# Optimization experiments

Hardware: AMD Instinct MI355X
Metric: run time of the kernel (lower is better)

## Reference

```python
import jax, jax.numpy as jnp
import numpy as np

ORDER = 2
C_IN = 32   # per-hop feature dim d
C_OUT = 64


def setup_inputs() -> dict:
    key = jax.random.key(0)
    k = jax.random.split(key, 6)
    b, num_n, num_m, d, t = 2, 512, 256, C_IN, 128
    feat_context = jax.random.normal(k[0], (b, num_n, d, t), dtype=jnp.float32)
    feat_target = jax.random.normal(k[1], (b, num_m, d, t), dtype=jnp.float32)
    adj = jax.random.uniform(k[2], (b, ORDER, num_m, num_n), dtype=jnp.float32)
    missing_mask_context = jax.random.randint(k[3], (b, t, num_n), 0, 2).astype(jnp.float32)
    c_cat = (ORDER + 1) * d  # 96
    W_mlp = jax.random.normal(k[4], (C_OUT, c_cat), dtype=jnp.float32) / np.sqrt(c_cat)
    b_mlp = jax.random.normal(k[5], (C_OUT,), dtype=jnp.float32) * 0.01
    return {"feat_context": feat_context, "feat_target": feat_target, "adj": adj,
            "missing_mask_context": missing_mask_context, "W_mlp": W_mlp, "b_mlp": b_mlp}


def _aggregate(fc_btnd, ft_btmd, adj_bmn, mask_btn):
    # mask out missing context nodes, per (batch, time)
    a = adj_bmn[:, None, :, :] * (1.0 - mask_btn[:, :, None, :])   # [b,t,m,n]
    norm = a / (jnp.sum(a, axis=-1, keepdims=True) + 1.0)          # [b,t,m,n]
    # residual + adjacency-weighted neighbor sum (batched matmul instead of [b,t,m,n,d] blow-up)
    agg = ft_btmd + jnp.einsum('btmn,btnd->btmd', norm, fc_btnd)   # [b,t,m,d]
    return agg


def reference(feat_context, feat_target, adj, missing_mask_context, W_mlp, b_mlp):
    # feat_context: [b,n,d,t], feat_target: [b,m,d,t], adj: [b,k,m,n], mask: [b,t,n]
    fc = jnp.transpose(feat_context, (0, 3, 1, 2))  # [b,t,n,d]
    ft = jnp.transpose(feat_target, (0, 3, 1, 2))   # [b,t,m,d]
    outs = [feat_target]
    for i in range(ORDER):
        agg = _aggregate(fc, ft, adj[:, i], missing_mask_context)      # [b,t,m,d]
        outs.append(jnp.transpose(agg, (0, 2, 3, 1)))                  # [b,m,d,t]
    out = jnp.concatenate(outs, axis=2)  # [b,m,(order+1)*d,t]
    # 1x1 conv over the feature channel dim + ReLU (dropout is identity at eval)
    y = jnp.einsum('bmct,oc->bmot', out, W_mlp) + b_mlp[None, None, :, None]
    return jax.nn.relu(y)  # [b,m,c_out,t]
```

## Files before the change

### kernel.cpp

```cpp
#include <hip/hip_runtime.h>
#include <cstdint>
#include <cstddef>


using shortx8 = __attribute__((ext_vector_type(8))) short;
using floatx4 = __attribute__((ext_vector_type(4))) float;

__device__ __forceinline__ float b2f(unsigned short u) {
    union { unsigned int i; float f; } v; v.i = ((unsigned int)u) << 16; return v.f;
}
__device__ __forceinline__ unsigned short f2b(float f) {
    union { float f; unsigned int i; } v; v.f = f;
    unsigned int x = v.i;
    return (unsigned short)((x + 0x7FFFu + ((x >> 16) & 1u)) >> 16);
}
__device__ __forceinline__ void gl_lds16(const unsigned short* g, unsigned short* l) {
    __builtin_amdgcn_global_load_lds(
        (const __attribute__((address_space(1))) unsigned int*)g,
        (__attribute__((address_space(3))) unsigned int*)l, 16, 0, 0);
}

__global__ void k_adj(const float* __restrict__ adj, const float* __restrict__ W,
                      unsigned short* __restrict__ adjb, unsigned short* __restrict__ Wb) {
    if (blockIdx.x == 512) {
        for (int e = threadIdx.x; e < 2048; e += 256) {
            int o = e >> 5, d = e & 31;
            float w1 = W[o * 96 + d], w2 = W[o * 96 + 32 + d], w3 = W[o * 96 + 64 + d];
            Wb[e]        = f2b(w1 + w2 + w3);
            Wb[2048 + e] = f2b(w2);
            Wb[4096 + e] = f2b(w3);
        }
        return;
    }
    int i4 = (blockIdx.x * 256 + threadIdx.x) * 4;
    float4 v = *(const float4*)(adj + i4);
    ushort4 o;
    o.x = f2b(v.x); o.y = f2b(v.y); o.z = f2b(v.z); o.w = f2b(v.w);
    *(ushort4*)(adjb + i4) = o;
}

__global__ void k_g(const float* __restrict__ fc, const float* __restrict__ mask,
                    unsigned short* __restrict__ gt) {
    const int jb = blockIdx.x, nb = blockIdx.y, b = blockIdx.z;
    const int tid = threadIdx.x;
    const int n0 = nb * 32;
    const int r = tid >> 3, c4 = (tid & 7) * 4;
    if (jb >= 128) {
        const int t0 = (jb - 128) * 32;
        float4 mv = *(const float4*)(mask + ((size_t)b * 128 + t0 + r) * 512 + n0 + c4);
        ushort4 o;
        o.x = f2b(1.f - mv.x); o.y = f2b(1.f - mv.y);
        o.z = f2b(1.f - mv.z); o.w = f2b(1.f - mv.w);
        *(ushort4*)(gt + ((size_t)b * 4224 + 4096 + t0 + r) * 512 + n0 + c4) = o;
        return;
    }
    const int j0 = jb * 32;
    const int t0 = j0 & 127;
    __shared__ float wls[32][33];
    __shared__ unsigned short tls[32][34];
    {
        float4 mv = *(const float4*)(mask + ((size_t)b * 128 + t0 + r) * 512 + n0 + c4);
        wls[r][c4 + 0] = 1.f - mv.x; wls[r][c4 + 1] = 1.f - mv.y;
        wls[r][c4 + 2] = 1.f - mv.z; wls[r][c4 + 3] = 1.f - mv.w;
    }
    float4 fv = *(const float4*)(fc + ((size_t)b * 512 + n0 + r) * 4096 + j0 + c4);
    __syncthreads();
    tls[c4 + 0][r] = f2b(fv.x * wls[c4 + 0][r]);
    tls[c4 + 1][r] = f2b(fv.y * wls[c4 + 1][r]);
    tls[c4 + 2][r] = f2b(fv.z * wls[c4 + 2][r]);
    tls[c4 + 3][r] = f2b(fv.w * wls[c4 + 3][r]);
    __syncthreads();
    ushort4 o;
    o.x = tls[r][c4 + 0]; o.y = tls[r][c4 + 1];
    o.z = tls[r][c4 + 2]; o.w = tls[r][c4 + 3];
    *(ushort4*)(gt + ((size_t)b * 4224 + j0 + r) * 512 + n0 + c4) = o;
}

__global__ void k_ft(const float* __restrict__ ft, unsigned short* __restrict__ ftT) {
    const int m = blockIdx.x, b = blockIdx.y;
    const int tid = threadIdx.x;
    __shared__ unsigned short l[32][136];
    const float* src = ft + ((size_t)(b * 256 + m) * 32) * 128;
    {
        const int d = tid >> 3, t0 = (tid & 7) * 16;
        float4 v0 = *(const float4*)(src + (size_t)d * 128 + t0);
        float4 v1 = *(const float4*)(src + (size_t)d * 128 + t0 + 4);
        float4 v2 = *(const float4*)(src + (size_t)d * 128 + t0 + 8);
        float4 v3 = *(const float4*)(src + (size_t)d * 128 + t0 + 12);
        unsigned short* p = &l[d][t0];
        p[0]  = f2b(v0.x); p[1]  = f2b(v0.y); p[2]  = f2b(v0.z); p[3]  = f2b(v0.w);
        p[4]  = f2b(v1.x); p[5]  = f2b(v1.y); p[6]  = f2b(v1.z); p[7]  = f2b(v1.w);
        p[8]  = f2b(v2.x); p[9]  = f2b(v2.y); p[10] = f2b(v2.z); p[11] = f2b(v2.w);
        p[12] = f2b(v3.x); p[13] = f2b(v3.y); p[14] = f2b(v3.z); p[15] = f2b(v3.w);
    }
    __syncthreads();
    {
        const int t = tid & 127, dh = (tid >> 7) * 16;
        unsigned short tmp[16];
        #pragma unroll
        for (int k = 0; k < 16; ++k) tmp[k] = l[dh + k][t];
        unsigned short* dst = ftT + ((size_t)(b * 256 + m) * 128 + t) * 32 + dh;
        *(shortx8*)(dst)     = *(const shortx8*)(tmp);
        *(shortx8*)(dst + 8) = *(const shortx8*)(tmp + 8);
    }
}

__launch_bounds__(256, 1)
__global__ void k_gemm(const unsigned short* __restrict__ adjb,
                       const unsigned short* __restrict__ gt,
                       unsigned short* __restrict__ ut,
                       unsigned short* __restrict__ sbuf) {
    const int jt = blockIdx.x, mt = blockIdx.y, bi = blockIdx.z;
    const int b = bi >> 1;
    const int tid = threadIdx.x;
    const int wave = tid >> 6, lane = tid & 63;
    const int l15 = lane & 15, quad = lane >> 4;
    const int wm = wave >> 1, wj = wave & 1;

    __shared__ __align__(16) unsigned short Al[128 * 32];
    __shared__ __align__(16) unsigned short Bl[128 * 32];

    const int srow = lane >> 2;
    const int skq  = (lane & 3) * 8;
    const unsigned short* Ag = adjb + ((size_t)bi * 256 + mt * 128) * 512;
    const unsigned short* Bgb = gt + (size_t)b * 4224 * 512;

    floatx4 acc[4][4];
    #pragma unroll
    for (int i = 0; i < 4; ++i)
        #pragma unroll
        for (int j = 0; j < 4; ++j) acc[i][j] = (floatx4){0.f, 0.f, 0.f, 0.f};

    for (int k0 = 0; k0 < 512; k0 += 32) {
        __syncthreads();
        #pragma unroll
        for (int rr = 0; rr < 2; ++rr) {
            const int ch = wave * 2 + rr;
            const int row = ch * 16 + srow;
            gl_lds16(Ag + (size_t)row * 512 + k0 + skq, &Al[ch * 512]);
            const int jrow = (jt < 32) ? ((row & 31) * 128 + jt * 4 + (row >> 5))
                                       : (4096 + row);
            gl_lds16(Bgb + (size_t)jrow * 512 + k0 + skq, &Bl[ch * 512]);
        }
        __syncthreads();

        shortx8 af[4], bf[4];
        #pragma unroll
        for (int i = 0; i < 4; ++i)
            af[i] = *(const shortx8*)&Al[(wm * 64 + i * 16 + l15) * 32 + quad * 8];
        #pragma unroll
        for (int j = 0; j < 4; ++j)
            bf[j] = *(const shortx8*)&Bl[(wj * 64 + j * 16 + l15) * 32 + quad * 8];
        #pragma unroll
        for (int i = 0; i < 4; ++i)
            #pragma unroll
            for (int j = 0; j < 4; ++j)
                acc[i][j] = __builtin_amdgcn_mfma_f32_16x16x32_bf16(af[i], bf[j], acc[i][j], 0, 0, 0);
    }

    if (jt < 32) {
        #pragma unroll
        for (int i = 0; i < 4; ++i)
            #pragma unroll
            for (int jj = 0; jj < 4; ++jj) {
                const int d_   = (jj & 1) * 16 + l15;
                const int tloc = wj * 2 + (jj >> 1);
                const int t_   = jt * 4 + tloc;
                #pragma unroll
                for (int reg = 0; reg < 4; ++reg) {
                    const int m_ = mt * 128 + wm * 64 + i * 16 + quad * 4 + reg;
                    ut[(((size_t)bi * 256 + m_) * 128 + t_) * 32 + d_] = f2b(acc[i][jj][reg]);
                }
            }
    } else {
        #pragma unroll
        for (int i = 0; i < 4; ++i)
            #pragma unroll
            for (int jj = 0; jj < 4; ++jj) {
                const int t_ = wj * 64 + jj * 16 + l15;
                #pragma unroll
                for (int reg = 0; reg < 4; ++reg) {
                    const int m_ = mt * 128 + wm * 64 + i * 16 + quad * 4 + reg;
                    sbuf[((size_t)bi * 256 + m_) * 128 + t_] = f2b(acc[i][jj][reg]);
                }
            }
    }
}

__launch_bounds__(256)
__global__ void k_mlp(const unsigned short* __restrict__ ftT, const unsigned short* __restrict__ ut,
                      const unsigned short* __restrict__ sbuf, const unsigned short* __restrict__ Wb,
                      const float* __restrict__ bias, float* __restrict__ y) {
    const int m = blockIdx.x, b = blockIdx.y;
    const int tid = threadIdx.x;
    const int wave = tid >> 6, lane = tid & 63;
    const int l15 = lane & 15, quad = lane >> 4;

    const size_t wrow = (size_t)(wave * 16 + l15) * 32 + quad * 8;
    shortx8 aw = *(const shortx8*)(Wb + wrow);
    shortx8 a2 = *(const shortx8*)(Wb + 2048 + wrow);
    shortx8 a3 = *(const shortx8*)(Wb + 4096 + wrow);
    float bv[4];
    #pragma unroll
    for (int r = 0; r < 4; ++r) bv[r] = bias[wave * 16 + quad * 4 + r];

    const unsigned short* fp = ftT + ((size_t)(b * 256 + m) * 128) * 32;
    const unsigned short* u0 = ut + ((size_t)((2 * b + 0) * 256 + m) * 128) * 32;
    const unsigned short* u1 = ut + ((size_t)((2 * b + 1) * 256 + m) * 128) * 32;
    const unsigned short* s0 = sbuf + ((size_t)(2 * b + 0) * 256 + m) * 128;
    const unsigned short* s1 = sbuf + ((size_t)(2 * b + 1) * 256 + m) * 128;
    float* yp = y + ((size_t)(b * 256 + m) * 64) * 128;

    #pragma unroll
    for (int tt = 0; tt < 8; ++tt) {
        const int t = tt * 16 + l15;
        shortx8 bf = *(const shortx8*)(fp + (size_t)t * 32 + quad * 8);
        shortx8 b0 = *(const shortx8*)(u0 + (size_t)t * 32 + quad * 8);
        shortx8 b1 = *(const shortx8*)(u1 + (size_t)t * 32 + quad * 8);
        floatx4 z = {0.f, 0.f, 0.f, 0.f};
        floatx4 cw = __builtin_amdgcn_mfma_f32_16x16x32_bf16(aw, bf, z, 0, 0, 0);
        floatx4 c2 = __builtin_amdgcn_mfma_f32_16x16x32_bf16(a2, b0, z, 0, 0, 0);
        floatx4 c3 = __builtin_amdgcn_mfma_f32_16x16x32_bf16(a3, b1, z, 0, 0, 0);
        float r0 = 1.f / (b2f(s0[t]) + 1.f);
        float r1 = 1.f / (b2f(s1[t]) + 1.f);
        #pragma unroll
        for (int r = 0; r < 4; ++r) {
            const int o = wave * 16 + quad * 4 + r;
            float v = cw[r] + r0 * c2[r] + r1 * c3[r] + bv[r];
            yp[(size_t)o * 128 + t] = v > 0.f ? v : 0.f;
        }
    }
}

extern "C" void kernel_launch(void* const* d_in, const int* in_sizes, int n_in,
                              void* d_out, int out_size, void* d_ws, size_t ws_size,
                              hipStream_t stream) {
    const float* fc   = (const float*)d_in[0];
    const float* ft   = (const float*)d_in[1];
    const float* adj  = (const float*)d_in[2];
    const float* mask = (const float*)d_in[3];
    const float* W    = (const float*)d_in[4];
    const float* bias = (const float*)d_in[5];
    float* y = (float*)d_out;

    unsigned short* gt   = (unsigned short*)d_ws;
    unsigned short* adjb = gt   + (size_t)2 * 4224 * 512;
    unsigned short* ut   = adjb + (size_t)4 * 256 * 512;
    unsigned short* sbuf = ut   + (size_t)4 * 256 * 128 * 32;
    unsigned short* ftT  = sbuf + (size_t)4 * 256 * 128;
    unsigned short* Wb   = ftT  + (size_t)2 * 256 * 128 * 32;

    k_adj <<<513, 256, 0, stream>>>(adj, W, adjb, Wb);
    k_g   <<<dim3(132, 16, 2), 256, 0, stream>>>(fc, mask, gt);
    k_ft  <<<dim3(256, 2), 256, 0, stream>>>(ft, ftT);
    k_gemm<<<dim3(33, 2, 4), 256, 0, stream>>>(adjb, gt, ut, sbuf);
    k_mlp <<<dim3(256, 2), 256, 0, stream>>>(ftT, ut, sbuf, Wb, bias, y);
}
```

Before: 113.2 us.

## Fuse prep kernels into one launch and double-buffer GEMM LDS with K=64

```diff
diff --git a/kernel.cpp b/kernel.cpp
--- a/kernel.cpp
+++ b/kernel.cpp
@@ -20,88 +20,90 @@
         (__attribute__((address_space(3))) unsigned int*)l, 16, 0, 0);
 }
 
-__global__ void k_adj(const float* __restrict__ adj, const float* __restrict__ W,
-                      unsigned short* __restrict__ adjb, unsigned short* __restrict__ Wb) {
-    if (blockIdx.x == 512) {
-        for (int e = threadIdx.x; e < 2048; e += 256) {
+__global__ void k_prep(const float* __restrict__ fc, const float* __restrict__ mask,
+                       const float* __restrict__ adj, const float* __restrict__ W,
+                       const float* __restrict__ ft,
+                       unsigned short* __restrict__ gt, unsigned short* __restrict__ adjb,
+                       unsigned short* __restrict__ Wb, unsigned short* __restrict__ ftT) {
+    const int tid = threadIdx.x;
+    __shared__ float wls[32][33];
+    __shared__ unsigned short tls[32][34];
+    __shared__ unsigned short ftl[32][136];
+
+    if (blockIdx.x < 4224) {
+        const int r_ = blockIdx.x;
+        const int jb = r_ % 132;
+        const int rem = r_ / 132;
+        const int nb = rem & 15, b = rem >> 4;
+        const int n0 = nb * 32;
+        const int r = tid >> 3, c4 = (tid & 7) * 4;
+        if (jb >= 128) {
+            const int t0 = (jb - 128) * 32;
+            float4 mv = *(const float4*)(mask + ((size_t)b * 128 + t0 + r) * 512 + n0 + c4);
+            ushort4 o;
+            o.x = f2b(1.f - mv.x); o.y = f2b(1.f - mv.y);
+            o.z = f2b(1.f - mv.z); o.w = f2b(1.f - mv.w);
+            *(ushort4*)(gt + ((size_t)b * 4224 + 4096 + t0 + r) * 512 + n0 + c4) = o;
+            return;
+        }
+        const int j0 = jb * 32;
+        const int t0 = j0 & 127;
+        {
+            float4 mv = *(const float4*)(mask + ((size_t)b * 128 + t0 + r) * 512 + n0 + c4);
+            wls[r][c4 + 0] = 1.f - mv.x; wls[r][c4 + 1] = 1.f - mv.y;
+            wls[r][c4 + 2] = 1.f - mv.z; wls[r][c4 + 3] = 1.f - mv.w;
+        }
+        float4 fv = *(const float4*)(fc + ((size_t)b * 512 + n0 + r) * 4096 + j0 + c4);
+        __syncthreads();
+        tls[c4 + 0][r] = f2b(fv.x * wls[c4 + 0][r]);
+        tls[c4 + 1][r] = f2b(fv.y * wls[c4 + 1][r]);
+        tls[c4 + 2][r] = f2b(fv.z * wls[c4 + 2][r]);
+        tls[c4 + 3][r] = f2b(fv.w * wls[c4 + 3][r]);
+        __syncthreads();
+        ushort4 o;
+        o.x = tls[r][c4 + 0]; o.y = tls[r][c4 + 1];
+        o.z = tls[r][c4 + 2]; o.w = tls[r][c4 + 3];
+        *(ushort4*)(gt + ((size_t)b * 4224 + j0 + r) * 512 + n0 + c4) = o;
+    } else if (blockIdx.x < 4736) {
+        int i4 = ((blockIdx.x - 4224) * 256 + tid) * 4;
+        float4 v = *(const float4*)(adj + i4);
+        ushort4 o;
+        o.x = f2b(v.x); o.y = f2b(v.y); o.z = f2b(v.z); o.w = f2b(v.w);
+        *(ushort4*)(adjb + i4) = o;
+    } else if (blockIdx.x == 4736) {
+        for (int e = tid; e < 2048; e += 256) {
             int o = e >> 5, d = e & 31;
             float w1 = W[o * 96 + d], w2 = W[o * 96 + 32 + d], w3 = W[o * 96 + 64 + d];
             Wb[e]        = f2b(w1 + w2 + w3);
             Wb[2048 + e] = f2b(w2);
             Wb[4096 + e] = f2b(w3);
         }
-        return;
-    }
-    int i4 = (blockIdx.x * 256 + threadIdx.x) * 4;
-    float4 v = *(const float4*)(adj + i4);
-    ushort4 o;
-    o.x = f2b(v.x); o.y = f2b(v.y); o.z = f2b(v.z); o.w = f2b(v.w);
-    *(ushort4*)(adjb + i4) = o;
-}
-
-__global__ void k_g(const float* __restrict__ fc, const float* __restrict__ mask,
-                    unsigned short* __restrict__ gt) {
-    const int jb = blockIdx.x, nb = blockIdx.y, b = blockIdx.z;
-    const int tid = threadIdx.x;
-    const int n0 = nb * 32;
-    const int r = tid >> 3, c4 = (tid & 7) * 4;
-    if (jb >= 128) {
-        const int t0 = (jb - 128) * 32;
-        float4 mv = *(const float4*)(mask + ((size_t)b * 128 + t0 + r) * 512 + n0 + c4);
-        ushort4 o;
-        o.x = f2b(1.f - mv.x); o.y = f2b(1.f - mv.y);
-        o.z = f2b(1.f - mv.z); o.w = f2b(1.f - mv.w);
-        *(ushort4*)(gt + ((size_t)b * 4224 + 4096 + t0 + r) * 512 + n0 + c4) = o;
-        return;
-    }
-    const int j0 = jb * 32;
-    const int t0 = j0 & 127;
-    __shared__ float wls[32][33];
-    __shared__ unsigned short tls[32][34];
-    {
-        float4 mv = *(const float4*)(mask + ((size_t)b * 128 + t0 + r) * 512 + n0 + c4);
-        wls[r][c4 + 0] = 1.f - mv.x; wls[r][c4 + 1] = 1.f - mv.y;
-        wls[r][c4 + 2] = 1.f - mv.z; wls[r][c4 + 3] = 1.f - mv.w;
-    }
-    float4 fv = *(const float4*)(fc + ((size_t)b * 512 + n0 + r) * 4096 + j0 + c4);
-    __syncthreads();
-    tls[c4 + 0][r] = f2b(fv.x * wls[c4 + 0][r]);
-    tls[c4 + 1][r] = f2b(fv.y * wls[c4 + 1][r]);
-    tls[c4 + 2][r] = f2b(fv.z * wls[c4 + 2][r]);
-    tls[c4 + 3][r] = f2b(fv.w * wls[c4 + 3][r]);
-    __syncthreads();
-    ushort4 o;
-    o.x = tls[r][c4 + 0]; o.y = tls[r][c4 + 1];
-    o.z = tls[r][c4 + 2]; o.w = tls[r][c4 + 3];
-    *(ushort4*)(gt + ((size_t)b * 4224 + j0 + r) * 512 + n0 + c4) = o;
-}
-
-__global__ void k_ft(const float* __restrict__ ft, unsigned short* __restrict__ ftT) {
-    const int m = blockIdx.x, b = blockIdx.y;
-    const int tid = threadIdx.x;
-    __shared__ unsigned short l[32][136];
-    const float* src = ft + ((size_t)(b * 256 + m) * 32) * 128;
-    {
-        const int d = tid >> 3, t0 = (tid & 7) * 16;
-        float4 v0 = *(const float4*)(src + (size_t)d * 128 + t0);
-        float4 v1 = *(const float4*)(src + (size_t)d * 128 + t0 + 4);
-        float4 v2 = *(const float4*)(src + (size_t)d * 128 + t0 + 8);
-        float4 v3 = *(const float4*)(src + (size_t)d * 128 + t0 + 12);
-        unsigned short* p = &l[d][t0];
-        p[0]  = f2b(v0.x); p[1]  = f2b(v0.y); p[2]  = f2b(v0.z); p[3]  = f2b(v0.w);
-        p[4]  = f2b(v1.x); p[5]  = f2b(v1.y); p[6]  = f2b(v1.z); p[7]  = f2b(v1.w);
-        p[8]  = f2b(v2.x); p[9]  = f2b(v2.y); p[10] = f2b(v2.z); p[11] = f2b(v2.w);
-        p[12] = f2b(v3.x); p[13] = f2b(v3.y); p[14] = f2b(v3.z); p[15] = f2b(v3.w);
-    }
-    __syncthreads();
-    {
-        const int t = tid & 127, dh = (tid >> 7) * 16;
-        unsigned short tmp[16];
-        #pragma unroll
-        for (int k = 0; k < 16; ++k) tmp[k] = l[dh + k][t];
-        unsigned short* dst = ftT + ((size_t)(b * 256 + m) * 128 + t) * 32 + dh;
-        *(shortx8*)(dst)     = *(const shortx8*)(tmp);
-        *(shortx8*)(dst + 8) = *(const shortx8*)(tmp + 8);
+    } else {
+        const int fb = blockIdx.x - 4737;
+        const int m = fb & 255, b = fb >> 8;
+        const float* src = ft + ((size_t)(b * 256 + m) * 32) * 128;
+        {
+            const int d = tid >> 3, t0 = (tid & 7) * 16;
+            float4 v0 = *(const float4*)(src + (size_t)d * 128 + t0);
+            float4 v1 = *(const float4*)(src + (size_t)d * 128 + t0 + 4);
+            float4 v2 = *(const float4*)(src + (size_t)d * 128 + t0 + 8);
+            float4 v3 = *(const float4*)(src + (size_t)d * 128 + t0 + 12);
+            unsigned short* p = &ftl[d][t0];
+            p[0]  = f2b(v0.x); p[1]  = f2b(v0.y); p[2]  = f2b(v0.z); p[3]  = f2b(v0.w);
+            p[4]  = f2b(v1.x); p[5]  = f2b(v1.y); p[6]  = f2b(v1.z); p[7]  = f2b(v1.w);
+            p[8]  = f2b(v2.x); p[9]  = f2b(v2.y); p[10] = f2b(v2.z); p[11] = f2b(v2.w);
+            p[12] = f2b(v3.x); p[13] = f2b(v3.y); p[14] = f2b(v3.z); p[15] = f2b(v3.w);
+        }
+        __syncthreads();
+        {
+            const int t = tid & 127, dh = (tid >> 7) * 16;
+            unsigned short tmp[16];
+            #pragma unroll
+            for (int k = 0; k < 16; ++k) tmp[k] = ftl[dh + k][t];
+            unsigned short* dst = ftT + ((size_t)(b * 256 + m) * 128 + t) * 32 + dh;
+            *(shortx8*)(dst)     = *(const shortx8*)(tmp);
+            *(shortx8*)(dst + 8) = *(const shortx8*)(tmp + 8);
+        }
     }
 }
 
@@ -117,13 +119,24 @@
     const int l15 = lane & 15, quad = lane >> 4;
     const int wm = wave >> 1, wj = wave & 1;
 
-    __shared__ __align__(16) unsigned short Al[128 * 32];
-    __shared__ __align__(16) unsigned short Bl[128 * 32];
-
-    const int srow = lane >> 2;
-    const int skq  = (lane & 3) * 8;
+    __shared__ __align__(16) unsigned short Al[2][128 * 64];
+    __shared__ __align__(16) unsigned short Bl[2][128 * 64];
+
+    const int srow = lane >> 3;
+    const int skq  = (lane & 7) * 8;
     const unsigned short* Ag = adjb + ((size_t)bi * 256 + mt * 128) * 512;
     const unsigned short* Bgb = gt + (size_t)b * 4224 * 512;
+
+    #define STAGE(buf, k0)                                                        \
+        _Pragma("unroll")                                                         \
+        for (int rr = 0; rr < 4; ++rr) {                                          \
+            const int ch = wave * 4 + rr;                                         \
+            const int row = ch * 8 + srow;                                        \
+            gl_lds16(Ag + (size_t)row * 512 + (k0) + skq, &Al[buf][ch * 512]);    \
+            const int jrow = (jt < 32) ? ((row & 31) * 128 + jt * 4 + (row >> 5)) \
+                                       : (4096 + row);                            \
+            gl_lds16(Bgb + (size_t)jrow * 512 + (k0) + skq, &Bl[buf][ch * 512]);  \
+        }
 
     floatx4 acc[4][4];
     #pragma unroll
@@ -131,32 +144,29 @@
         #pragma unroll
         for (int j = 0; j < 4; ++j) acc[i][j] = (floatx4){0.f, 0.f, 0.f, 0.f};
 
-    for (int k0 = 0; k0 < 512; k0 += 32) {
-        __syncthreads();
-        #pragma unroll
-        for (int rr = 0; rr < 2; ++rr) {
-            const int ch = wave * 2 + rr;
-            const int row = ch * 16 + srow;
-            gl_lds16(Ag + (size_t)row * 512 + k0 + skq, &Al[ch * 512]);
-            const int jrow = (jt < 32) ? ((row & 31) * 128 + jt * 4 + (row >> 5))
-                                       : (4096 + row);
-            gl_lds16(Bgb + (size_t)jrow * 512 + k0 + skq, &Bl[ch * 512]);
-        }
-        __syncthreads();
-
-        shortx8 af[4], bf[4];
-        #pragma unroll
-        for (int i = 0; i < 4; ++i)
-            af[i] = *(const shortx8*)&Al[(wm * 64 + i * 16 + l15) * 32 + quad * 8];
-        #pragma unroll
-        for (int j = 0; j < 4; ++j)
-            bf[j] = *(const shortx8*)&Bl[(wj * 64 + j * 16 + l15) * 32 + quad * 8];
-        #pragma unroll
-        for (int i = 0; i < 4; ++i)
+    STAGE(0, 0)
+    int cur = 0;
+    for (int it = 0; it < 8; ++it) {
+        __syncthreads();
+        if (it < 7) { STAGE(cur ^ 1, (it + 1) * 64) }
+        #pragma unroll
+        for (int ks = 0; ks < 2; ++ks) {
+            shortx8 af[4], bf[4];
+            #pragma unroll
+            for (int i = 0; i < 4; ++i)
+                af[i] = *(const shortx8*)&Al[cur][(wm * 64 + i * 16 + l15) * 64 + ks * 32 + quad * 8];
             #pragma unroll
             for (int j = 0; j < 4; ++j)
-                acc[i][j] = __builtin_amdgcn_mfma_f32_16x16x32_bf16(af[i], bf[j], acc[i][j], 0, 0, 0);
-    }
+                bf[j] = *(const shortx8*)&Bl[cur][(wj * 64 + j * 16 + l15) * 64 + ks * 32 + quad * 8];
+            #pragma unroll
+            for (int i = 0; i < 4; ++i)
+                #pragma unroll
+                for (int j = 0; j < 4; ++j)
+                    acc[i][j] = __builtin_amdgcn_mfma_f32_16x16x32_bf16(af[i], bf[j], acc[i][j], 0, 0, 0);
+        }
+        cur ^= 1;
+    }
+    #undef STAGE
 
     if (jt < 32) {
         #pragma unroll
@@ -250,9 +260,7 @@
     unsigned short* ftT  = sbuf + (size_t)4 * 256 * 128;
     unsigned short* Wb   = ftT  + (size_t)2 * 256 * 128 * 32;
 
-    k_adj <<<513, 256, 0, stream>>>(adj, W, adjb, Wb);
-    k_g   <<<dim3(132, 16, 2), 256, 0, stream>>>(fc, mask, gt);
-    k_ft  <<<dim3(256, 2), 256, 0, stream>>>(ft, ftT);
+    k_prep<<<5249, 256, 0, stream>>>(fc, mask, adj, W, ft, gt, adjb, Wb, ftT);
     k_gemm<<<dim3(33, 2, 4), 256, 0, stream>>>(adjb, gt, ut, sbuf);
     k_mlp <<<dim3(256, 2), 256, 0, stream>>>(ftT, ut, sbuf, Wb, bias, y);
 }
```

After: 110.9 us. 1.02x faster.
